# Kernel tuning notes

Hardware: AMD Instinct MI355X
Metric: run time of the kernel (lower is better)

The kernel has to match this reference:

```python
import jax, jax.numpy as jnp
import numpy as np

B, T, D = 4, 2048, 1024
H = 16
HD = D // H  # 64


def setup_inputs() -> dict:
    key = jax.random.key(0)
    ks = jax.random.split(key, 7)
    scale = 1.0 / np.sqrt(D)
    x = jax.random.normal(ks[0], (B, T, D), dtype=jnp.float32)
    # per-head projection weights, stacked over heads: [H, D, HD]
    Wq = jax.random.normal(ks[1], (H, D, HD), dtype=jnp.float32) * scale
    Wk = jax.random.normal(ks[2], (H, D, HD), dtype=jnp.float32) * scale
    Wv = jax.random.normal(ks[3], (H, D, HD), dtype=jnp.float32) * scale
    s_raw = jnp.zeros((H,), dtype=jnp.float32)  # learnable ssmax scale per head
    proj_W = jax.random.normal(ks[4], (D, D), dtype=jnp.float32) * scale
    proj_b = jax.random.normal(ks[5], (D,), dtype=jnp.float32) * 0.01
    return {"x": x, "Wq": Wq, "Wk": Wk, "Wv": Wv, "s_raw": s_raw,
            "proj_W": proj_W, "proj_b": proj_b}


def reference(x, Wq, Wk, Wv, s_raw, proj_W, proj_b):
    # per-head q/k/v: [B, H, T, HD]
    q = jnp.einsum('btd,hde->bhte', x, Wq)
    k = jnp.einsum('btd,hde->bhte', x, Wk)
    v = jnp.einsum('btd,hde->bhte', x, Wv)

    # ssmax: q scaled by softplus(s) * log(position index, 1-based)
    logn = jnp.log(jnp.arange(1, T + 1, dtype=x.dtype))  # [T]
    s = jax.nn.softplus(s_raw)  # [H]
    q = q * (s[None, :, None, None] * logn[None, None, :, None])

    scores = jnp.einsum('bhte,bhse->bhts', q, k) * (HD ** -0.5)
    causal = jnp.tril(jnp.ones((T, T), dtype=bool))
    scores = jnp.where(causal[None, None], scores, -jnp.inf)
    w = jax.nn.softmax(scores, axis=-1)

    out = jnp.einsum('bhts,bhse->bhte', w, v)          # [B, H, T, HD]
    out = out.transpose(0, 2, 1, 3).reshape(B, T, D)    # concat heads
    return out @ proj_W.T + proj_b
```

## Files before the change

kernel.cpp:

```cpp
#include <hip/hip_runtime.h>
#include <hip/hip_bf16.h>

#define Bv 4
#define Tv 2048
#define Dv 1024
#define Hv 16
#define HDv 64
#define Mv (Bv*Tv)

typedef __hip_bfloat16 bf16;
typedef short s8v __attribute__((ext_vector_type(8)));
typedef float f4v __attribute__((ext_vector_type(4)));
typedef float f16a __attribute__((ext_vector_type(16)));

__device__ __forceinline__ unsigned short f2us(float x){
    bf16 h = __float2bfloat16(x);
    return *reinterpret_cast<unsigned short*>(&h);
}
__device__ __forceinline__ unsigned int pack2(float a, float b){
    return (unsigned int)f2us(a) | ((unsigned int)f2us(b) << 16);
}
__device__ __forceinline__ void glds16(const unsigned short* g, unsigned short* lds_base){
    __builtin_amdgcn_global_load_lds(
        (const __attribute__((address_space(1))) unsigned int*)g,
        (__attribute__((address_space(3))) unsigned int*)lds_base, 16, 0, 0);
}

__global__ void cvt_kernel(const float* __restrict__ src,
                           unsigned short* __restrict__ dst, int n4) {
    int i = blockIdx.x * 256 + threadIdx.x;
    if (i < n4) {
        float4 f = *(const float4*)(src + (size_t)i * 4);
        ushort4 o;
        o.x = f2us(f.x); o.y = f2us(f.y); o.z = f2us(f.z); o.w = f2us(f.w);
        *(ushort4*)(dst + (size_t)i * 4) = o;
    }
}

__global__ __launch_bounds__(256) void wt_kernel(
    const float* __restrict__ Wq, const float* __restrict__ Wk,
    const float* __restrict__ Wv, unsigned short* __restrict__ Wt)
{
    const int dt  = blockIdx.x;
    const int h   = blockIdx.y;
    const int sel = blockIdx.z;
    const float* W = (sel == 0) ? Wq : ((sel == 1) ? Wk : Wv);
    const float* Wh = W + (size_t)h * Dv * HDv;
    __shared__ float Tf[64][65];
    const int tid = threadIdx.x;
    for (int l = 0; l < 16; ++l) {
        int idx = tid + l * 256;
        int r = idx >> 6, e = idx & 63;
        Tf[r][e] = Wh[(size_t)(dt * 64 + r) * HDv + e];
    }
    __syncthreads();
    unsigned short* out = Wt + ((size_t)sel * Hv + h) * HDv * Dv;
    for (int l = 0; l < 16; ++l) {
        int idx = tid + l * 256;
        int e = idx >> 6, d = idx & 63;
        out[(size_t)e * Dv + dt * 64 + d] = f2us(Tf[d][e]);
    }
}

__global__ __launch_bounds__(256) void qkv_big(
    const unsigned short* __restrict__ xb, const unsigned short* __restrict__ Wc,
    const float* __restrict__ s_raw,
    unsigned short* __restrict__ q, unsigned short* __restrict__ k,
    unsigned short* __restrict__ vT)
{
    const int bm = blockIdx.x;
    const int bn = blockIdx.y;
    const int tid = threadIdx.x;
    const int w = tid >> 6, lane = tid & 63;
    const int n16 = lane & 15, quad = lane >> 4;
    const int wm = w >> 1, wn = w & 1;

    __shared__ __align__(16) unsigned short As[128 * 64];
    __shared__ __align__(16) unsigned short Bs[128 * 64];

    f4v acc[4][4];
    f4v zero = {0.f, 0.f, 0.f, 0.f};
    #pragma unroll
    for (int i = 0; i < 4; ++i)
        #pragma unroll
        for (int j = 0; j < 4; ++j) acc[i][j] = zero;

    const int row0 = bm * 128, col0 = bn * 128;
    const int lr = lane >> 3, lc = (lane & 7) * 8;

    for (int k0 = 0; k0 < Dv; k0 += 64) {
        __syncthreads();
        #pragma unroll
        for (int i = 0; i < 4; ++i) {
            int rb = w * 32 + i * 8;
            glds16(xb + (size_t)(row0 + rb + lr) * Dv + k0 + lc, &As[rb * 64]);
            glds16(Wc + (size_t)(col0 + rb + lr) * Dv + k0 + lc, &Bs[rb * 64]);
        }
        __syncthreads();
        #pragma unroll
        for (int ks = 0; ks < 2; ++ks) {
            s8v bfr[4];
            #pragma unroll
            for (int ni = 0; ni < 4; ++ni)
                bfr[ni] = *(const s8v*)(&Bs[(wn * 64 + ni * 16 + n16) * 64 + ks * 32 + quad * 8]);
            #pragma unroll
            for (int mi = 0; mi < 4; ++mi) {
                s8v afr = *(const s8v*)(&As[(wm * 64 + mi * 16 + n16) * 64 + ks * 32 + quad * 8]);
                #pragma unroll
                for (int ni = 0; ni < 4; ++ni)
                    acc[mi][ni] = __builtin_amdgcn_mfma_f32_16x16x32_bf16(afr, bfr[ni], acc[mi][ni], 0, 0, 0);
            }
        }
    }

    #pragma unroll
    for (int ni = 0; ni < 4; ++ni) {
        int n = col0 + wn * 64 + ni * 16 + n16;
        int sel = n >> 10, h = (n >> 6) & 15, e = n & 63;
        if (sel == 2) {
            #pragma unroll
            for (int mi = 0; mi < 4; ++mi) {
                int row = row0 + wm * 64 + mi * 16 + quad * 4;
                int bb_ = row >> 11, t = row & (Tv - 1);
                ushort4 o4;
                o4.x = f2us(acc[mi][ni][0]); o4.y = f2us(acc[mi][ni][1]);
                o4.z = f2us(acc[mi][ni][2]); o4.w = f2us(acc[mi][ni][3]);
                *(ushort4*)(vT + ((size_t)(bb_ * Hv + h) * HDv + e) * Tv + t) = o4;
            }
        } else {
            unsigned short* out = (sel == 0) ? q : k;
            float sc_h = (sel == 0) ? log1pf(expf(s_raw[h])) * 0.125f : 1.0f;
            #pragma unroll
            for (int mi = 0; mi < 4; ++mi) {
                #pragma unroll
                for (int r = 0; r < 4; ++r) {
                    int row = row0 + wm * 64 + mi * 16 + quad * 4 + r;
                    int bb_ = row >> 11, t = row & (Tv - 1);
                    float rs = (sel == 0) ? sc_h * logf((float)(t + 1)) : 1.0f;
                    out[((size_t)(bb_ * Hv + h) * Tv + t) * HDv + e] = f2us(acc[mi][ni][r] * rs);
                }
            }
        }
    }
}

__global__ __launch_bounds__(256) void attn_mfma(
    const unsigned short* __restrict__ q, const unsigned short* __restrict__ k,
    const unsigned short* __restrict__ vT, unsigned short* __restrict__ attn)
{
    const int bh = blockIdx.y;
    const int b = bh >> 4, h = bh & 15;
    const int tid = threadIdx.x;
    const int w = tid >> 6, lane = tid & 63;
    const int l31 = lane & 31, hi = lane >> 5;

    __shared__ __align__(16) unsigned short Ks[128][72];
    __shared__ __align__(16) unsigned short VTs[64][136];

    const size_t hb = (size_t)(b * Hv + h) * Tv * HDv;
    const unsigned short* kb = k + hb;
    const unsigned short* vb = vT + hb;

    for (int phase = 0; phase < 2; ++phase) {
        const int qt = phase ? (15 - (int)blockIdx.x) : (int)blockIdx.x;
        const int qstrip = qt * 128 + w * 32;
        const int myq = qstrip + l31;

        s8v qf[4];
        #pragma unroll
        for (int ks = 0; ks < 4; ++ks)
            qf[ks] = *(const s8v*)(q + hb + (size_t)myq * HDv + ks * 16 + hi * 8);

        f16a st[4], ot0, ot1;
        #pragma unroll
        for (int i = 0; i < 16; ++i) { ot0[i] = 0.f; ot1[i] = 0.f; }
        float lrun = 0.f;

        for (int ss = 0; ss <= qt; ++ss) {
            const int s0 = ss * 128;
            __syncthreads();
            #pragma unroll
            for (int l = 0; l < 4; ++l) {
                int idx = tid + l * 256;
                int r = idx >> 3, c = (idx & 7) * 8;
                *(ulonglong2*)(&Ks[r][c]) =
                    *(const ulonglong2*)(kb + (size_t)(s0 + r) * HDv + c);
            }
            #pragma unroll
            for (int l = 0; l < 4; ++l) {
                int idx = tid + l * 256;
                int e = idx >> 4, c = (idx & 15) * 8;
                *(ulonglong2*)(&VTs[e][c]) =
                    *(const ulonglong2*)(vb + (size_t)e * Tv + s0 + c);
            }
            __syncthreads();

            #pragma unroll
            for (int mt = 0; mt < 4; ++mt)
                #pragma unroll
                for (int i = 0; i < 16; ++i) st[mt][i] = 0.f;
            #pragma unroll
            for (int ks = 0; ks < 4; ++ks) {
                #pragma unroll
                for (int mt = 0; mt < 4; ++mt) {
                    s8v a = *(const s8v*)(&Ks[32 * mt + l31][ks * 16 + hi * 8]);
                    st[mt] = __builtin_amdgcn_mfma_f32_32x32x16_bf16(a, qf[ks], st[mt], 0, 0, 0);
                }
            }
            if (s0 + 127 > qstrip) {
                #pragma unroll
                for (int mt = 0; mt < 4; ++mt)
                    #pragma unroll
                    for (int reg = 0; reg < 16; ++reg) {
                        int srow = (reg & 3) + 8 * (reg >> 2) + 4 * hi;
                        if (s0 + 32 * mt + srow > myq) st[mt][reg] = -1e30f;
                    }
            }
            float lsum = 0.f;
            #pragma unroll
            for (int mt = 0; mt < 4; ++mt)
                #pragma unroll
                for (int i = 0; i < 16; ++i) {
                    st[mt][i] = __expf(st[mt][i]);
                    lsum += st[mt][i];
                }
            lrun += lsum;

            #pragma unroll
            for (int half = 0; half < 2; ++half) {
                unsigned int pk[16];
                #pragma unroll
                for (int g = 0; g < 4; ++g) {
                    pk[2*g]       = pack2(st[2*half][4*g],     st[2*half][4*g+1]);
                    pk[2*g+1]     = pack2(st[2*half][4*g+2],   st[2*half][4*g+3]);
                    pk[8+2*g]     = pack2(st[2*half+1][4*g],   st[2*half+1][4*g+1]);
                    pk[8+2*g+1]   = pack2(st[2*half+1][4*g+2], st[2*half+1][4*g+3]);
                }
                #pragma unroll
                for (int ks4 = 0; ks4 < 4; ++ks4) {
                    const int ks = half * 4 + ks4;
                    const int base = (ks4 >> 1) * 8 + (ks4 & 1) * 4;
                    unsigned int v0 = hi ? pk[base]     : pk[base + 2];
                    unsigned int v1 = hi ? pk[base + 1] : pk[base + 3];
                    unsigned int r0 = (unsigned int)__shfl_xor((int)v0, 32);
                    unsigned int r1 = (unsigned int)__shfl_xor((int)v1, 32);
                    union { s8v v; unsigned int d[4]; } bf;
                    bf.d[0] = hi ? r0 : pk[base];
                    bf.d[1] = hi ? r1 : pk[base + 1];
                    bf.d[2] = hi ? pk[base + 2] : r0;
                    bf.d[3] = hi ? pk[base + 3] : r1;
                    s8v a0 = *(const s8v*)(&VTs[l31][ks * 16 + hi * 8]);
                    s8v a1 = *(const s8v*)(&VTs[32 + l31][ks * 16 + hi * 8]);
                    ot0 = __builtin_amdgcn_mfma_f32_32x32x16_bf16(a0, bf.v, ot0, 0, 0, 0);
                    ot1 = __builtin_amdgcn_mfma_f32_32x32x16_bf16(a1, bf.v, ot1, 0, 0, 0);
                }
            }
        }

        float ltot = lrun + __shfl_xor(lrun, 32);
        float inv = 1.0f / ltot;
        size_t obase = ((size_t)(b * Tv) + myq) * Dv + h * HDv;
        #pragma unroll
        for (int g = 0; g < 4; ++g) {
            ushort4 o4;
            o4.x = f2us(ot0[4*g]   * inv); o4.y = f2us(ot0[4*g+1] * inv);
            o4.z = f2us(ot0[4*g+2] * inv); o4.w = f2us(ot0[4*g+3] * inv);
            *(ushort4*)(attn + obase + 8 * g + 4 * hi) = o4;
            o4.x = f2us(ot1[4*g]   * inv); o4.y = f2us(ot1[4*g+1] * inv);
            o4.z = f2us(ot1[4*g+2] * inv); o4.w = f2us(ot1[4*g+3] * inv);
            *(ushort4*)(attn + obase + 32 + 8 * g + 4 * hi) = o4;
        }
    }
}

__global__ __launch_bounds__(256) void proj_big(
    const unsigned short* __restrict__ attn, const unsigned short* __restrict__ Wb,
    const float* __restrict__ bias, float* __restrict__ out)
{
    const int bm = blockIdx.x;
    const int bn = blockIdx.y;
    const int tid = threadIdx.x;
    const int w = tid >> 6, lane = tid & 63;
    const int n16 = lane & 15, quad = lane >> 4;
    const int wm = w >> 1, wn = w & 1;

    __shared__ __align__(16) unsigned short As[128 * 64];
    __shared__ __align__(16) unsigned short Bs[128 * 64];

    f4v acc[4][4];
    f4v zero = {0.f, 0.f, 0.f, 0.f};
    #pragma unroll
    for (int i = 0; i < 4; ++i)
        #pragma unroll
        for (int j = 0; j < 4; ++j) acc[i][j] = zero;

    const int row0 = bm * 128, col0 = bn * 128;
    const int lr = lane >> 3, lc = (lane & 7) * 8;

    for (int k0 = 0; k0 < Dv; k0 += 64) {
        __syncthreads();
        #pragma unroll
        for (int i = 0; i < 4; ++i) {
            int rb = w * 32 + i * 8;
            glds16(attn + (size_t)(row0 + rb + lr) * Dv + k0 + lc, &As[rb * 64]);
            glds16(Wb   + (size_t)(col0 + rb + lr) * Dv + k0 + lc, &Bs[rb * 64]);
        }
        __syncthreads();
        #pragma unroll
        for (int ks = 0; ks < 2; ++ks) {
            s8v bfr[4];
            #pragma unroll
            for (int ni = 0; ni < 4; ++ni)
                bfr[ni] = *(const s8v*)(&Bs[(wn * 64 + ni * 16 + n16) * 64 + ks * 32 + quad * 8]);
            #pragma unroll
            for (int mi = 0; mi < 4; ++mi) {
                s8v afr = *(const s8v*)(&As[(wm * 64 + mi * 16 + n16) * 64 + ks * 32 + quad * 8]);
                #pragma unroll
                for (int ni = 0; ni < 4; ++ni)
                    acc[mi][ni] = __builtin_amdgcn_mfma_f32_16x16x32_bf16(afr, bfr[ni], acc[mi][ni], 0, 0, 0);
            }
        }
    }
    #pragma unroll
    for (int ni = 0; ni < 4; ++ni) {
        int n = col0 + wn * 64 + ni * 16 + n16;
        float bn_ = bias[n];
        #pragma unroll
        for (int mi = 0; mi < 4; ++mi) {
            #pragma unroll
            for (int r = 0; r < 4; ++r) {
                int m = row0 + wm * 64 + mi * 16 + quad * 4 + r;
                out[(size_t)m * Dv + n] = acc[mi][ni][r] + bn_;
            }
        }
    }
}

extern "C" void kernel_launch(void* const* d_in, const int* in_sizes, int n_in,
                              void* d_out, int out_size, void* d_ws, size_t ws_size,
                              hipStream_t stream) {
    const float* x     = (const float*)d_in[0];
    const float* Wq    = (const float*)d_in[1];
    const float* Wk    = (const float*)d_in[2];
    const float* Wv    = (const float*)d_in[3];
    const float* s_raw = (const float*)d_in[4];
    const float* projW = (const float*)d_in[5];
    const float* projb = (const float*)d_in[6];
    float* out = (float*)d_out;

    const size_t nx  = (size_t)Mv * Dv;
    const size_t nqk = (size_t)Bv * Hv * Tv * HDv;
    unsigned short* x_bf = (unsigned short*)d_ws;
    unsigned short* qb   = x_bf + nx;
    unsigned short* kb   = qb + nqk;
    unsigned short* vTb  = kb + nqk;
    unsigned short* Wt   = vTb + nqk;
    unsigned short* Wpb  = Wt + (size_t)3 * Hv * HDv * Dv;
    unsigned short* attn = x_bf;

    cvt_kernel<<<(int)(nx / 4 / 256), 256, 0, stream>>>(x, x_bf, (int)(nx / 4));
    cvt_kernel<<<(int)((size_t)Dv * Dv / 4 / 256), 256, 0, stream>>>(projW, Wpb, Dv * Dv / 4);
    wt_kernel<<<dim3(16, 16, 3), 256, 0, stream>>>(Wq, Wk, Wv, Wt);
    qkv_big<<<dim3(Mv / 128, 3072 / 128), 256, 0, stream>>>(x_bf, Wt, s_raw, qb, kb, vTb);
    attn_mfma<<<dim3(8, Bv * Hv), 256, 0, stream>>>(qb, kb, vTb, attn);
    proj_big<<<dim3(Mv / 128, Dv / 128), 256, 0, stream>>>(attn, Wpb, projb, out);
}
```

Before: 283.3 us.

## Rewrite QKV GEMM as 256x256 tile, 8-wave, double-buffered ping-pong pipeline

Result: faster. 268.9 us (-5.1%).

```diff
diff --git a/kernel.cpp b/kernel.cpp
--- a/kernel.cpp
+++ b/kernel.cpp
@@ -62,82 +62,150 @@
     }
 }
 
-__global__ __launch_bounds__(256) void qkv_big(
+__global__ __launch_bounds__(512, 2) void qkv_8ph(
     const unsigned short* __restrict__ xb, const unsigned short* __restrict__ Wc,
     const float* __restrict__ s_raw,
     unsigned short* __restrict__ q, unsigned short* __restrict__ k,
     unsigned short* __restrict__ vT)
 {
+    extern __shared__ unsigned short smem[];
     const int bm = blockIdx.x;
     const int bn = blockIdx.y;
     const int tid = threadIdx.x;
     const int w = tid >> 6, lane = tid & 63;
-    const int n16 = lane & 15, quad = lane >> 4;
-    const int wm = w >> 1, wn = w & 1;
-
-    __shared__ __align__(16) unsigned short As[128 * 64];
-    __shared__ __align__(16) unsigned short Bs[128 * 64];
-
-    f4v acc[4][4];
+    const int wm = w >> 2, wn = w & 3;
+    const int n16 = lane & 15, quad = lane >> 4, l7 = lane & 7;
+
+    const int row0 = bm * 256, col0 = bn * 256;
+
+    const int sr = lane >> 3;
+    const int sc = ((lane & 7) ^ (sr & 7)) * 8;
+
+    f4v acc[8][4];
     f4v zero = {0.f, 0.f, 0.f, 0.f};
     #pragma unroll
-    for (int i = 0; i < 4; ++i)
+    for (int i = 0; i < 8; ++i)
         #pragma unroll
         for (int j = 0; j < 4; ++j) acc[i][j] = zero;
 
-    const int row0 = bm * 128, col0 = bn * 128;
-    const int lr = lane >> 3, lc = (lane & 7) * 8;
-
-    for (int k0 = 0; k0 < Dv; k0 += 64) {
-        __syncthreads();
-        #pragma unroll
-        for (int i = 0; i < 4; ++i) {
-            int rb = w * 32 + i * 8;
-            glds16(xb + (size_t)(row0 + rb + lr) * Dv + k0 + lc, &As[rb * 64]);
-            glds16(Wc + (size_t)(col0 + rb + lr) * Dv + k0 + lc, &Bs[rb * 64]);
-        }
-        __syncthreads();
-        #pragma unroll
-        for (int ks = 0; ks < 2; ++ks) {
-            s8v bfr[4];
-            #pragma unroll
-            for (int ni = 0; ni < 4; ++ni)
-                bfr[ni] = *(const s8v*)(&Bs[(wn * 64 + ni * 16 + n16) * 64 + ks * 32 + quad * 8]);
-            #pragma unroll
-            for (int mi = 0; mi < 4; ++mi) {
-                s8v afr = *(const s8v*)(&As[(wm * 64 + mi * 16 + n16) * 64 + ks * 32 + quad * 8]);
-                #pragma unroll
-                for (int ni = 0; ni < 4; ++ni)
-                    acc[mi][ni] = __builtin_amdgcn_mfma_f32_16x16x32_bf16(afr, bfr[ni], acc[mi][ni], 0, 0, 0);
-            }
-        }
-    }
-
-    #pragma unroll
-    for (int ni = 0; ni < 4; ++ni) {
-        int n = col0 + wn * 64 + ni * 16 + n16;
-        int sel = n >> 10, h = (n >> 6) & 15, e = n & 63;
-        if (sel == 2) {
-            #pragma unroll
-            for (int mi = 0; mi < 4; ++mi) {
-                int row = row0 + wm * 64 + mi * 16 + quad * 4;
+    s8v Ar[8][2];
+    s8v Br[4][2];
+
+    auto stageA = [&](int b, int h, int tk){
+        const unsigned short* g = xb + ((size_t)(row0 + h*128 + w*16 + sr)) * Dv + tk*64 + sc;
+        unsigned short* l = smem + b*32768 + h*8192 + w*1024;
+        glds16(g, l);
+        glds16(g + 8*Dv, l + 512);
+    };
+    auto stageB = [&](int b, int h, int tk){
+        const unsigned short* g = Wc + ((size_t)(col0 + h*128 + w*16 + sr)) * Dv + tk*64 + sc;
+        unsigned short* l = smem + b*32768 + 16384 + h*8192 + w*1024;
+        glds16(g, l);
+        glds16(g + 8*Dv, l + 512);
+    };
+    auto readA = [&](int b, int mh){
+        #pragma unroll
+        for (int mi = 0; mi < 4; ++mi)
+            #pragma unroll
+            for (int kk = 0; kk < 2; ++kk)
+                Ar[mh*4+mi][kk] = *(const s8v*)(smem + b*32768 + wm*8192
+                    + ((mh*4+mi)*16 + n16) * 64 + (((kk*4 + quad) ^ l7) * 8));
+    };
+    auto readB = [&](int b, int nh){
+        #pragma unroll
+        for (int ni = 0; ni < 2; ++ni)
+            #pragma unroll
+            for (int kk = 0; kk < 2; ++kk)
+                Br[nh*2+ni][kk] = *(const s8v*)(smem + b*32768 + 16384 + (wn>>1)*8192
+                    + ((wn&1)*64 + (nh*2+ni)*16 + n16) * 64 + (((kk*4 + quad) ^ l7) * 8));
+    };
+    auto quadMM = [&](int mh, int nh){
+        #pragma unroll
+        for (int kk = 0; kk < 2; ++kk)
+            #pragma unroll
+            for (int mi = 0; mi < 4; ++mi)
+                #pragma unroll
+                for (int ni = 0; ni < 2; ++ni)
+                    acc[mh*4+mi][nh*2+ni] = __builtin_amdgcn_mfma_f32_16x16x32_bf16(
+                        Ar[mh*4+mi][kk], Br[nh*2+ni][kk], acc[mh*4+mi][nh*2+ni], 0, 0, 0);
+    };
+
+    stageA(0,0,0); stageA(0,1,0); stageB(0,0,0); stageB(0,1,0);
+    stageA(1,0,1); stageA(1,1,1); stageB(1,0,1); stageB(1,1,1);
+    asm volatile("s_waitcnt vmcnt(8)" ::: "memory");
+    __builtin_amdgcn_s_barrier();
+
+    #pragma unroll 1
+    for (int it = 0; it < 8; ++it) {
+        const int t2 = (2*it + 2) & 15, t3 = (2*it + 3) & 15;
+        readA(0,0); readB(0,0);
+        __builtin_amdgcn_s_barrier();
+        __builtin_amdgcn_s_setprio(1); quadMM(0,0); __builtin_amdgcn_s_setprio(0);
+        __builtin_amdgcn_s_barrier();
+        readB(0,1); readA(0,1);
+        __builtin_amdgcn_s_barrier();
+        __builtin_amdgcn_s_setprio(1); quadMM(0,1); __builtin_amdgcn_s_setprio(0);
+        asm volatile("s_waitcnt lgkmcnt(0)" ::: "memory");
+        __builtin_amdgcn_s_barrier();
+        stageA(0,0,t2);
+        __builtin_amdgcn_s_barrier();
+        __builtin_amdgcn_s_setprio(1); quadMM(1,0); __builtin_amdgcn_s_setprio(0);
+        __builtin_amdgcn_s_barrier();
+        stageA(0,1,t2);
+        __builtin_amdgcn_s_barrier();
+        __builtin_amdgcn_s_setprio(1); quadMM(1,1); __builtin_amdgcn_s_setprio(0);
+        asm volatile("s_waitcnt vmcnt(4)" ::: "memory");
+        __builtin_amdgcn_s_barrier();
+        readA(1,0); readB(1,0); stageB(0,0,t2);
+        __builtin_amdgcn_s_barrier();
+        __builtin_amdgcn_s_setprio(1); quadMM(0,0); __builtin_amdgcn_s_setprio(0);
+        __builtin_amdgcn_s_barrier();
+        readB(1,1); readA(1,1); stageB(0,1,t2);
+        __builtin_amdgcn_s_barrier();
+        __builtin_amdgcn_s_setprio(1); quadMM(0,1); __builtin_amdgcn_s_setprio(0);
+        asm volatile("s_waitcnt lgkmcnt(0)" ::: "memory");
+        __builtin_amdgcn_s_barrier();
+        stageA(1,0,t3); stageA(1,1,t3);
+        __builtin_amdgcn_s_barrier();
+        __builtin_amdgcn_s_setprio(1); quadMM(1,0); __builtin_amdgcn_s_setprio(0);
+        __builtin_amdgcn_s_barrier();
+        stageB(1,0,t3); stageB(1,1,t3);
+        __builtin_amdgcn_s_barrier();
+        __builtin_amdgcn_s_setprio(1); quadMM(1,1); __builtin_amdgcn_s_setprio(0);
+        asm volatile("s_waitcnt vmcnt(8)" ::: "memory");
+        __builtin_amdgcn_s_barrier();
+    }
+
+    const int sel = bn >> 2;
+    const int h = (bn * 4 + wn) & 15;
+    if (sel == 2) {
+        #pragma unroll
+        for (int ni = 0; ni < 4; ++ni) {
+            int e = ni * 16 + n16;
+            #pragma unroll
+            for (int mi = 0; mi < 8; ++mi) {
+                int row = row0 + wm * 128 + mi * 16 + quad * 4;
                 int bb_ = row >> 11, t = row & (Tv - 1);
                 ushort4 o4;
                 o4.x = f2us(acc[mi][ni][0]); o4.y = f2us(acc[mi][ni][1]);
                 o4.z = f2us(acc[mi][ni][2]); o4.w = f2us(acc[mi][ni][3]);
                 *(ushort4*)(vT + ((size_t)(bb_ * Hv + h) * HDv + e) * Tv + t) = o4;
             }
-        } else {
-            unsigned short* out = (sel == 0) ? q : k;
-            float sc_h = (sel == 0) ? log1pf(expf(s_raw[h])) * 0.125f : 1.0f;
-            #pragma unroll
-            for (int mi = 0; mi < 4; ++mi) {
+        }
+    } else {
+        unsigned short* outp = (sel == 0) ? q : k;
+        const float sc_h = (sel == 0) ? log1pf(expf(s_raw[h])) * 0.125f : 1.0f;
+        #pragma unroll
+        for (int ni = 0; ni < 4; ++ni) {
+            int e = ni * 16 + n16;
+            #pragma unroll
+            for (int mi = 0; mi < 8; ++mi) {
                 #pragma unroll
                 for (int r = 0; r < 4; ++r) {
-                    int row = row0 + wm * 64 + mi * 16 + quad * 4 + r;
+                    int row = row0 + wm * 128 + mi * 16 + quad * 4 + r;
                     int bb_ = row >> 11, t = row & (Tv - 1);
-                    float rs = (sel == 0) ? sc_h * logf((float)(t + 1)) : 1.0f;
-                    out[((size_t)(bb_ * Hv + h) * Tv + t) * HDv + e] = f2us(acc[mi][ni][r] * rs);
+                    float rs = (sel == 0) ? sc_h * __logf((float)(t + 1)) : 1.0f;
+                    outp[((size_t)(bb_ * Hv + h) * Tv + t) * HDv + e] = f2us(acc[mi][ni][r] * rs);
                 }
             }
         }
@@ -358,10 +426,17 @@
     unsigned short* Wpb  = Wt + (size_t)3 * Hv * HDv * Dv;
     unsigned short* attn = x_bf;
 
+    static int cfg = 0;
+    if (!cfg) {
+        (void)hipFuncSetAttribute((const void*)qkv_8ph,
+                                  hipFuncAttributeMaxDynamicSharedMemorySize, 131072);
+        cfg = 1;
+    }
+
     cvt_kernel<<<(int)(nx / 4 / 256), 256, 0, stream>>>(x, x_bf, (int)(nx / 4));
     cvt_kernel<<<(int)((size_t)Dv * Dv / 4 / 256), 256, 0, stream>>>(projW, Wpb, Dv * Dv / 4);
     wt_kernel<<<dim3(16, 16, 3), 256, 0, stream>>>(Wq, Wk, Wv, Wt);
-    qkv_big<<<dim3(Mv / 128, 3072 / 128), 256, 0, stream>>>(x_bf, Wt, s_raw, qb, kb, vTb);
+    qkv_8ph<<<dim3(Mv / 256, 3072 / 256), 512, 131072, stream>>>(x_bf, Wt, s_raw, qb, kb, vTb);
     attn_mfma<<<dim3(8, Bv * Hv), 256, 0, stream>>>(qb, kb, vTb, attn);
     proj_big<<<dim3(Mv / 128, Dv / 128), 256, 0, stream>>>(attn, Wpb, projb, out);
 }
```
